# Kernel optimization log

Hardware: AMD Instinct MI355X
Metric: run time of the kernel (lower is better)

The kernel has to match this reference:

```python
import jax, jax.numpy as jnp
import numpy as np

B, S, D = 4, 4096, 1024

def setup_inputs() -> dict:
    key = jax.random.key(0)
    ks = jax.random.split(key, 7)
    scale = 1.0 / np.sqrt(D)
    X  = jax.random.normal(ks[0], (B, S, D), dtype=jnp.float32)
    Wq = jax.random.normal(ks[1], (D, D), dtype=jnp.float32) * scale
    bq = jnp.zeros((D,), dtype=jnp.float32)
    Wk = jax.random.normal(ks[2], (D, D), dtype=jnp.float32) * scale
    bk = jnp.zeros((D,), dtype=jnp.float32)
    Wv = jax.random.normal(ks[3], (D, D), dtype=jnp.float32) * scale
    bv = jnp.zeros((D,), dtype=jnp.float32)
    return {"X": X, "Wq": Wq, "bq": bq, "Wk": Wk, "bk": bk, "Wv": Wv, "bv": bv}

def reference(X, Wq, bq, Wk, bk, Wv, bv):
    # Linear projections (torch Linear: x @ W.T + b; here W stored as [D_in, D_out])
    Q = jnp.einsum('bsd,de->bse', X, Wq) + bq
    K = jnp.einsum('bsd,de->bse', X, Wk) + bk
    V = jnp.einsum('bsd,de->bse', X, Wv) + bv
    inv_sqrt_d = 1.0 / jnp.sqrt(jnp.float32(X.shape[-1]))
    scores = jnp.einsum('bqd,bkd->bqk', Q, K) * inv_sqrt_d  # [B,S,S]
    weights = jax.nn.sigmoid(scores)  # elementwise, no row normalization
    return jnp.einsum('bqk,bkd->bqd', weights, V)
```

## Files before the change

kernel.cpp:

```cpp
#include <hip/hip_runtime.h>
#include <hip/hip_bf16.h>

typedef __bf16 bf16_t;
typedef bf16_t bf16x8 __attribute__((ext_vector_type(8)));
typedef float f32x4 __attribute__((ext_vector_type(4)));

constexpr int BM = 128, BN = 128, BK = 32;
constexpr int D_DIM = 1024;
constexpr int S_DIM = 4096;
constexpr int B_DIM = 4;

__global__ void cast_f32_bf16(const float* __restrict__ in, bf16_t* __restrict__ out) {
  size_t i = ((size_t)blockIdx.x * blockDim.x + threadIdx.x) * 8;
  float4 a = *(const float4*)(in + i);
  float4 b = *(const float4*)(in + i + 4);
  bf16x8 o;
  o[0] = (bf16_t)a.x; o[1] = (bf16_t)a.y; o[2] = (bf16_t)a.z; o[3] = (bf16_t)a.w;
  o[4] = (bf16_t)b.x; o[5] = (bf16_t)b.y; o[6] = (bf16_t)b.z; o[7] = (bf16_t)b.w;
  *(bf16x8*)(out + i) = o;
}

__global__ void transpose_cast_1024(const float* __restrict__ in, bf16_t* __restrict__ out) {
  __shared__ float t[32][33];
  int x0 = blockIdx.x * 32, y0 = blockIdx.y * 32;
#pragma unroll
  for (int i = 0; i < 32; i += 8)
    t[threadIdx.y + i][threadIdx.x] =
        in[(size_t)(y0 + threadIdx.y + i) * D_DIM + (x0 + threadIdx.x)];
  __syncthreads();
#pragma unroll
  for (int i = 0; i < 32; i += 8)
    out[(size_t)(x0 + threadIdx.y + i) * D_DIM + (y0 + threadIdx.x)] =
        (bf16_t)t[threadIdx.x][threadIdx.y + i];
}

__device__ __forceinline__ void stage128x32(const bf16_t* __restrict__ g, int ld,
                                            bf16_t* lds, int tid) {
  int w = tid >> 6;
  int r = tid >> 2;
  int c = (tid & 3) * 8;
  const bf16_t* g0 = g + (size_t)r * ld + c;
  const bf16_t* g1 = g0 + (size_t)64 * ld;
  bf16_t* l0 = lds + w * 512;
  __builtin_amdgcn_global_load_lds((const __attribute__((address_space(1))) void*)g0,
                                   (__attribute__((address_space(3))) void*)l0, 16, 0, 0);
  __builtin_amdgcn_global_load_lds((const __attribute__((address_space(1))) void*)g1,
                                   (__attribute__((address_space(3))) void*)(l0 + 2048), 16, 0, 0);
}

template <int EPI, bool SWAP>
__global__ __launch_bounds__(256) void gemm_bt(
    const bf16_t* __restrict__ A, const bf16_t* __restrict__ Bt,
    void* __restrict__ C0, void* __restrict__ C1, void* __restrict__ C2,
    const float* __restrict__ b0, const float* __restrict__ b1, const float* __restrict__ b2,
    int K, int lda, int ldb, int ldc, float scale,
    size_t sA, size_t sB, size_t sC) {
  __shared__ bf16_t As[2 * BM * BK];
  __shared__ bf16_t Bs[2 * BN * BK];
  const int tid = threadIdx.x;
  const int lane = tid & 63;
  const int w = tid >> 6;
  const int wr = (w >> 1) * 64;
  const int wc = (w & 1) * 64;
  const int fm = lane & 15;
  const int fko = (lane >> 4) * 8;

  const int bx = SWAP ? blockIdx.y : blockIdx.x;
  const int by = SWAP ? blockIdx.x : blockIdx.y;

  const bf16_t* Ag = A + (size_t)blockIdx.z * sA + (size_t)by * BM * lda;
  const bf16_t* Bg = Bt + (size_t)blockIdx.z * sB + (size_t)bx * BN * ldb;

  f32x4 acc[4][4] = {};

  for (int k0 = 0; k0 < K; k0 += 2 * BK) {
    stage128x32(Ag + k0, lda, As, tid);
    stage128x32(Ag + k0 + BK, lda, As + BM * BK, tid);
    stage128x32(Bg + k0, ldb, Bs, tid);
    stage128x32(Bg + k0 + BK, ldb, Bs + BN * BK, tid);
    __syncthreads();
#pragma unroll
    for (int h = 0; h < 2; ++h) {
      const bf16_t* as = As + h * BM * BK;
      const bf16_t* bs = Bs + h * BN * BK;
      bf16x8 af[4], bfr[4];
#pragma unroll
      for (int i = 0; i < 4; ++i)
        af[i] = *(const bf16x8*)&as[(wr + i * 16 + fm) * BK + fko];
#pragma unroll
      for (int j = 0; j < 4; ++j)
        bfr[j] = *(const bf16x8*)&bs[(wc + j * 16 + fm) * BK + fko];
#pragma unroll
      for (int i = 0; i < 4; ++i)
#pragma unroll
        for (int j = 0; j < 4; ++j)
          acc[i][j] = __builtin_amdgcn_mfma_f32_16x16x32_bf16(af[i], bfr[j], acc[i][j], 0, 0, 0);
    }
    __syncthreads();
  }

  const int row0 = by * BM + wr + (lane >> 4) * 4;
  const int col0 = bx * BN + wc + fm;

  if constexpr (EPI == 0) {
    const int seg = (bx * BN) >> 10;
    const float* bias = (seg == 0) ? b0 : (seg == 1) ? b1 : b2;
#pragma unroll
    for (int i = 0; i < 4; ++i) {
#pragma unroll
      for (int j = 0; j < 4; ++j) {
        const int n = col0 + j * 16;
        const int nl = n & 1023;
        const float bv = bias[nl];
#pragma unroll
        for (int r = 0; r < 4; ++r) {
          const int m = row0 + i * 16 + r;
          float v = acc[i][j][r] + bv;
          if (seg < 2) {
            bf16_t* C = (bf16_t*)(seg == 0 ? C0 : C1);
            C[(size_t)m * D_DIM + nl] = (bf16_t)v;
          } else {
            bf16_t* C = (bf16_t*)C2;
            C[((size_t)(m >> 12) << 22) + (size_t)nl * S_DIM + (m & (S_DIM - 1))] = (bf16_t)v;
          }
        }
      }
    }
  } else {
#pragma unroll
    for (int i = 0; i < 4; ++i) {
#pragma unroll
      for (int j = 0; j < 4; ++j) {
        const int n = col0 + j * 16;
#pragma unroll
        for (int r = 0; r < 4; ++r) {
          const int m = row0 + i * 16 + r;
          float v = acc[i][j][r];
          if constexpr (EPI == 2) {
            bf16_t* C = (bf16_t*)C0 + (size_t)blockIdx.z * sC;
            float s = 1.0f / (1.0f + __expf(-v * scale));
            C[(size_t)m * ldc + n] = (bf16_t)s;
          } else {
            float* C = (float*)C0 + (size_t)blockIdx.z * sC;
            C[(size_t)m * ldc + n] = v;
          }
        }
      }
    }
  }
}

extern "C" void kernel_launch(void* const* d_in, const int* in_sizes, int n_in,
                              void* d_out, int out_size, void* d_ws, size_t ws_size,
                              hipStream_t stream) {
  const float* X  = (const float*)d_in[0];
  const float* Wq = (const float*)d_in[1];
  const float* bq = (const float*)d_in[2];
  const float* Wk = (const float*)d_in[3];
  const float* bk = (const float*)d_in[4];
  const float* Wv = (const float*)d_in[5];
  const float* bv = (const float*)d_in[6];
  float* out = (float*)d_out;

  const int M = B_DIM * S_DIM;
  const size_t SD = (size_t)S_DIM * D_DIM;
  const size_t E  = (size_t)M * D_DIM;
  const size_t PE1 = (size_t)S_DIM * S_DIM;
  const size_t WE = (size_t)D_DIM * D_DIM;

  size_t need4 = (4 * PE1 + 3 * E + 3 * WE) * sizeof(bf16_t);
  const int PB = (ws_size >= need4) ? 4 : 1;
  const size_t psz = (size_t)PB * PE1;

  bf16_t* ws = (bf16_t*)d_ws;
  bf16_t* P   = ws;
  bf16_t* Xb  = ws;
  bf16_t* Qb  = ws + psz;
  bf16_t* Kb  = Qb + E;
  bf16_t* Vt  = Kb + E;
  bf16_t* Wt  = Vt + E;

  cast_f32_bf16<<<dim3((unsigned)(E / 8 / 256)), dim3(256), 0, stream>>>(X, Xb);

  dim3 tg(D_DIM / 32, D_DIM / 32), tb(32, 8);
  transpose_cast_1024<<<tg, tb, 0, stream>>>(Wq, Wt);
  transpose_cast_1024<<<tg, tb, 0, stream>>>(Wk, Wt + WE);
  transpose_cast_1024<<<tg, tb, 0, stream>>>(Wv, Wt + 2 * WE);

  dim3 pg(3 * D_DIM / BN, M / BM, 1);
  gemm_bt<0, false><<<pg, 256, 0, stream>>>(Xb, Wt, Qb, Kb, Vt, bq, bk, bv,
                                            D_DIM, D_DIM, D_DIM, D_DIM, 1.0f, 0, 0, 0);

  const float scale = 0.03125f;
  for (int b0 = 0; b0 < B_DIM; b0 += PB) {
    dim3 sg(S_DIM / BN, S_DIM / BM, PB);
    gemm_bt<2, false><<<sg, 256, 0, stream>>>(Qb + (size_t)b0 * SD, Kb + (size_t)b0 * SD, P,
                                              nullptr, nullptr, nullptr, nullptr, nullptr,
                                              D_DIM, D_DIM, D_DIM, S_DIM, scale,
                                              SD, SD, PE1);
    dim3 vg(S_DIM / BM, D_DIM / BN, PB);
    gemm_bt<3, true><<<vg, 256, 0, stream>>>(P, Vt + (size_t)b0 * SD, out + (size_t)b0 * SD,
                                             nullptr, nullptr, nullptr, nullptr, nullptr,
                                             S_DIM, S_DIM, S_DIM, D_DIM, 1.0f,
                                             PE1, SD, SD);
  }
}
```

Before: 633.2 us.

## Store Q and K in FP8 and compute scores with FP8 MFMA

The projection epilogue now quantizes Q and K to FP8 (e4m3) bytes instead of bf16, while V stays bf16. A new score GEMM kernel reads these FP8 tiles and uses fp8 MFMA instructions before applying the sigmoid. The aim is to halve the operand bytes loaded for the QK^T product and use the FP8 matrix path. In exchange, the scores lose precision, the projection epilogue writes single bytes, and the batch chunk for the score buffer drops from 4 to 2, which means more kernel launches.

```diff
diff --git a/kernel.cpp b/kernel.cpp
--- a/kernel.cpp
+++ b/kernel.cpp
@@ -4,6 +4,9 @@
 typedef __bf16 bf16_t;
 typedef bf16_t bf16x8 __attribute__((ext_vector_type(8)));
 typedef float f32x4 __attribute__((ext_vector_type(4)));
+
+#define GASP const __attribute__((address_space(1))) void*
+#define LASP __attribute__((address_space(3))) void*
 
 constexpr int BM = 128, BN = 128, BK = 32;
 constexpr int D_DIM = 1024;
@@ -34,18 +37,15 @@
         (bf16_t)t[threadIdx.x][threadIdx.y + i];
 }
 
-__device__ __forceinline__ void stage128x32(const bf16_t* __restrict__ g, int ld,
-                                            bf16_t* lds, int tid) {
-  int w = tid >> 6;
+__device__ __forceinline__ void stage128x64B(const char* __restrict__ g, int ldb,
+                                             char* lds, int tid) {
   int r = tid >> 2;
-  int c = (tid & 3) * 8;
-  const bf16_t* g0 = g + (size_t)r * ld + c;
-  const bf16_t* g1 = g0 + (size_t)64 * ld;
-  bf16_t* l0 = lds + w * 512;
-  __builtin_amdgcn_global_load_lds((const __attribute__((address_space(1))) void*)g0,
-                                   (__attribute__((address_space(3))) void*)l0, 16, 0, 0);
-  __builtin_amdgcn_global_load_lds((const __attribute__((address_space(1))) void*)g1,
-                                   (__attribute__((address_space(3))) void*)(l0 + 2048), 16, 0, 0);
+  int c = (tid & 3) * 16;
+  const char* g0 = g + (size_t)r * ldb + c;
+  const char* g1 = g0 + (size_t)64 * ldb;
+  char* l0 = lds + (tid >> 6) * 1024;
+  __builtin_amdgcn_global_load_lds((GASP)g0, (LASP)l0, 16, 0, 0);
+  __builtin_amdgcn_global_load_lds((GASP)g1, (LASP)(l0 + 4096), 16, 0, 0);
 }
 
 template <int EPI, bool SWAP>
@@ -53,7 +53,7 @@
     const bf16_t* __restrict__ A, const bf16_t* __restrict__ Bt,
     void* __restrict__ C0, void* __restrict__ C1, void* __restrict__ C2,
     const float* __restrict__ b0, const float* __restrict__ b1, const float* __restrict__ b2,
-    int K, int lda, int ldb, int ldc, float scale,
+    int K, int lda, int ldb, int ldc,
     size_t sA, size_t sB, size_t sC) {
   __shared__ bf16_t As[2 * BM * BK];
   __shared__ bf16_t Bs[2 * BN * BK];
@@ -74,10 +74,10 @@
   f32x4 acc[4][4] = {};
 
   for (int k0 = 0; k0 < K; k0 += 2 * BK) {
-    stage128x32(Ag + k0, lda, As, tid);
-    stage128x32(Ag + k0 + BK, lda, As + BM * BK, tid);
-    stage128x32(Bg + k0, ldb, Bs, tid);
-    stage128x32(Bg + k0 + BK, ldb, Bs + BN * BK, tid);
+    stage128x64B((const char*)(Ag + k0), lda * 2, (char*)As, tid);
+    stage128x64B((const char*)(Ag + k0 + BK), lda * 2, (char*)(As + BM * BK), tid);
+    stage128x64B((const char*)(Bg + k0), ldb * 2, (char*)Bs, tid);
+    stage128x64B((const char*)(Bg + k0 + BK), ldb * 2, (char*)(Bs + BN * BK), tid);
     __syncthreads();
 #pragma unroll
     for (int h = 0; h < 2; ++h) {
@@ -117,11 +117,12 @@
           const int m = row0 + i * 16 + r;
           float v = acc[i][j][r] + bv;
           if (seg < 2) {
-            bf16_t* C = (bf16_t*)(seg == 0 ? C0 : C1);
-            C[(size_t)m * D_DIM + nl] = (bf16_t)v;
+            unsigned char q8 =
+                (unsigned char)(__builtin_amdgcn_cvt_pk_fp8_f32(v, v, 0, false) & 0xff);
+            ((unsigned char*)(seg == 0 ? C0 : C1))[(size_t)m * D_DIM + nl] = q8;
           } else {
-            bf16_t* C = (bf16_t*)C2;
-            C[((size_t)(m >> 12) << 22) + (size_t)nl * S_DIM + (m & (S_DIM - 1))] = (bf16_t)v;
+            ((bf16_t*)C2)[((size_t)(m >> 12) << 22) + (size_t)nl * S_DIM + (m & (S_DIM - 1))] =
+                (bf16_t)v;
           }
         }
       }
@@ -135,19 +136,80 @@
 #pragma unroll
         for (int r = 0; r < 4; ++r) {
           const int m = row0 + i * 16 + r;
-          float v = acc[i][j][r];
-          if constexpr (EPI == 2) {
-            bf16_t* C = (bf16_t*)C0 + (size_t)blockIdx.z * sC;
-            float s = 1.0f / (1.0f + __expf(-v * scale));
-            C[(size_t)m * ldc + n] = (bf16_t)s;
-          } else {
-            float* C = (float*)C0 + (size_t)blockIdx.z * sC;
-            C[(size_t)m * ldc + n] = v;
-          }
+          ((float*)C0 + (size_t)blockIdx.z * sC)[(size_t)m * ldc + n] = acc[i][j][r];
         }
       }
     }
   }
+}
+
+__global__ __launch_bounds__(256) void gemm_fp8_sig(
+    const unsigned char* __restrict__ Q, const unsigned char* __restrict__ Kt,
+    bf16_t* __restrict__ P, float scale, size_t sA, size_t sB, size_t sC) {
+  __shared__ char As[2 * 128 * 64];
+  __shared__ char Bs[2 * 128 * 64];
+  const int tid = threadIdx.x;
+  const int lane = tid & 63;
+  const int w = tid >> 6;
+  const int wr = (w >> 1) * 64;
+  const int wc = (w & 1) * 64;
+  const int fm = lane & 15;
+  const int ko8 = (lane >> 4) * 8;
+
+  const unsigned char* Qg = Q + (size_t)blockIdx.z * sA + (size_t)blockIdx.y * BM * D_DIM;
+  const unsigned char* Kg = Kt + (size_t)blockIdx.z * sB + (size_t)blockIdx.x * BN * D_DIM;
+
+  f32x4 acc[4][4] = {};
+
+  for (int k0 = 0; k0 < D_DIM; k0 += 128) {
+    stage128x64B((const char*)(Qg + k0), D_DIM, As, tid);
+    stage128x64B((const char*)(Qg + k0 + 64), D_DIM, As + 8192, tid);
+    stage128x64B((const char*)(Kg + k0), D_DIM, Bs, tid);
+    stage128x64B((const char*)(Kg + k0 + 64), D_DIM, Bs + 8192, tid);
+    __syncthreads();
+#pragma unroll
+    for (int h = 0; h < 2; ++h) {
+      const char* as = As + h * 8192;
+      const char* bs = Bs + h * 8192;
+      long a0[4], a1[4], bq0[4], bq1[4];
+#pragma unroll
+      for (int i = 0; i < 4; ++i) {
+        const char* r = &as[(wr + i * 16 + fm) * 64 + ko8];
+        a0[i] = *(const long*)r;
+        a1[i] = *(const long*)(r + 32);
+      }
+#pragma unroll
+      for (int j = 0; j < 4; ++j) {
+        const char* r = &bs[(wc + j * 16 + fm) * 64 + ko8];
+        bq0[j] = *(const long*)r;
+        bq1[j] = *(const long*)(r + 32);
+      }
+#pragma unroll
+      for (int i = 0; i < 4; ++i)
+#pragma unroll
+        for (int j = 0; j < 4; ++j) {
+          acc[i][j] = __builtin_amdgcn_mfma_f32_16x16x32_fp8_fp8(a0[i], bq0[j], acc[i][j], 0, 0, 0);
+          acc[i][j] = __builtin_amdgcn_mfma_f32_16x16x32_fp8_fp8(a1[i], bq1[j], acc[i][j], 0, 0, 0);
+        }
+    }
+    __syncthreads();
+  }
+
+  const int row0 = blockIdx.y * BM + wr + (lane >> 4) * 4;
+  const int col0 = blockIdx.x * BN + wc + fm;
+  bf16_t* C = P + (size_t)blockIdx.z * sC;
+#pragma unroll
+  for (int i = 0; i < 4; ++i)
+#pragma unroll
+    for (int j = 0; j < 4; ++j) {
+      const int n = col0 + j * 16;
+#pragma unroll
+      for (int r = 0; r < 4; ++r) {
+        const int m = row0 + i * 16 + r;
+        float s = 1.0f / (1.0f + __expf(-acc[i][j][r] * scale));
+        C[(size_t)m * S_DIM + n] = (bf16_t)s;
+      }
+    }
 }
 
 extern "C" void kernel_launch(void* const* d_in, const int* in_sizes, int n_in,
@@ -168,17 +230,19 @@
   const size_t PE1 = (size_t)S_DIM * S_DIM;
   const size_t WE = (size_t)D_DIM * D_DIM;
 
-  size_t need4 = (4 * PE1 + 3 * E + 3 * WE) * sizeof(bf16_t);
-  const int PB = (ws_size >= need4) ? 4 : 1;
-  const size_t psz = (size_t)PB * PE1;
-
-  bf16_t* ws = (bf16_t*)d_ws;
-  bf16_t* P   = ws;
-  bf16_t* Xb  = ws;
-  bf16_t* Qb  = ws + psz;
-  bf16_t* Kb  = Qb + E;
-  bf16_t* Vt  = Kb + E;
-  bf16_t* Wt  = Vt + E;
+  auto need = [&](int pb) {
+    return (size_t)pb * PE1 * 2 + 2 * E  + E * 2  + 3 * WE * 2 ;
+  };
+  const int PB = (ws_size >= need(2)) ? 2 : 1;
+  const size_t pbytes = (size_t)PB * PE1 * 2;
+
+  char* wsb = (char*)d_ws;
+  bf16_t* P  = (bf16_t*)wsb;
+  bf16_t* Xb = (bf16_t*)wsb;
+  unsigned char* Qb = (unsigned char*)(wsb + pbytes);
+  unsigned char* Kb = Qb + E;
+  bf16_t* Vt = (bf16_t*)(Kb + E);
+  bf16_t* Wt = Vt + E;
 
   cast_f32_bf16<<<dim3((unsigned)(E / 8 / 256)), dim3(256), 0, stream>>>(X, Xb);
 
@@ -189,19 +253,17 @@
 
   dim3 pg(3 * D_DIM / BN, M / BM, 1);
   gemm_bt<0, false><<<pg, 256, 0, stream>>>(Xb, Wt, Qb, Kb, Vt, bq, bk, bv,
-                                            D_DIM, D_DIM, D_DIM, D_DIM, 1.0f, 0, 0, 0);
+                                            D_DIM, D_DIM, D_DIM, D_DIM, 0, 0, 0);
 
   const float scale = 0.03125f;
   for (int b0 = 0; b0 < B_DIM; b0 += PB) {
     dim3 sg(S_DIM / BN, S_DIM / BM, PB);
-    gemm_bt<2, false><<<sg, 256, 0, stream>>>(Qb + (size_t)b0 * SD, Kb + (size_t)b0 * SD, P,
-                                              nullptr, nullptr, nullptr, nullptr, nullptr,
-                                              D_DIM, D_DIM, D_DIM, S_DIM, scale,
-                                              SD, SD, PE1);
+    gemm_fp8_sig<<<sg, 256, 0, stream>>>(Qb + (size_t)b0 * SD, Kb + (size_t)b0 * SD, P,
+                                         scale, SD, SD, PE1);
     dim3 vg(S_DIM / BM, D_DIM / BN, PB);
     gemm_bt<3, true><<<vg, 256, 0, stream>>>(P, Vt + (size_t)b0 * SD, out + (size_t)b0 * SD,
                                              nullptr, nullptr, nullptr, nullptr, nullptr,
-                                             S_DIM, S_DIM, S_DIM, D_DIM, 1.0f,
+                                             S_DIM, S_DIM, S_DIM, D_DIM,
                                              PE1, SD, SD);
   }
 }
```

New measurement: 692.0 us. 1.09x slower.
